# Kernel tuning notes

Measured on AMD Instinct MI355X. Metric: run time of the kernel, lower is better.

Reference implementation:

```python
import jax, jax.numpy as jnp
import numpy as np

N_NODES = 10000
N_EDGES = 640000
MODEL_DIM = 128
HIDDEN = [128, 128]


def setup_inputs() -> dict:
    key = jax.random.key(0)
    ks = jax.random.split(key, 10)
    node_feature = jax.random.normal(ks[0], (N_NODES, MODEL_DIM), dtype=jnp.float32)
    src = jax.random.randint(ks[1], (N_EDGES,), 0, N_NODES, dtype=jnp.int32)
    dst = jax.random.randint(ks[2], (N_EDGES,), 0, N_NODES, dtype=jnp.int32)
    in_dim = 2 * MODEL_DIM  # concat(aggregated_message, node_feature)
    # MLP: in_dim -> 128 -> 128 -> MODEL_DIM, ReLU between hidden layers
    W1 = jax.random.normal(ks[3], (in_dim, HIDDEN[0]), dtype=jnp.float32) / np.sqrt(in_dim)
    b1 = jnp.zeros((HIDDEN[0],), dtype=jnp.float32)
    W2 = jax.random.normal(ks[4], (HIDDEN[0], HIDDEN[1]), dtype=jnp.float32) / np.sqrt(HIDDEN[0])
    b2 = jnp.zeros((HIDDEN[1],), dtype=jnp.float32)
    W3 = jax.random.normal(ks[5], (HIDDEN[1], MODEL_DIM), dtype=jnp.float32) / np.sqrt(HIDDEN[1])
    b3 = jnp.zeros((MODEL_DIM,), dtype=jnp.float32)
    return {"node_feature": node_feature, "src": src, "dst": dst,
            "W1": W1, "b1": b1, "W2": W2, "b2": b2, "W3": W3, "b3": b3}


def reference(node_feature, src, dst, W1, b1, W2, b2, W3, b3):
    # message: gather src node features along edges  [E, D]
    # reduce: sum messages into dst nodes            [N, D]
    agg = jax.ops.segment_sum(node_feature[src], dst, num_segments=N_NODES)
    # apply_node_function_yes_neighbor: concat(aggregated_message, node_feature) -> MLP
    x = jnp.concatenate([agg, node_feature], axis=-1)  # [N, 2D]
    h = jax.nn.relu(x @ W1 + b1)
    h = jax.nn.relu(h @ W2 + b2)
    out = h @ W3 + b3  # [N, D]
    return out
```

## Files before the change

kernel.cpp:

```cpp
#include <hip/hip_runtime.h>
#include <hip/hip_bf16.h>

#define MODEL_D 128
#define CHUNK_SHIFT 13
#define CHUNK_SZ (1 << CHUNK_SHIFT)
#define CAPN 160
#define LDS_HIST 10240

typedef unsigned short ushort_t;
typedef unsigned int uint_t;
typedef __attribute__((ext_vector_type(8))) short short8v;
typedef __attribute__((ext_vector_type(4))) float f32x4;

static __device__ __forceinline__ ushort_t f2b(float v) {
    __hip_bfloat16 h = __float2bfloat16(v);
    return *reinterpret_cast<ushort_t*>(&h);
}

static __device__ __forceinline__ void acc8(float* acc, uint4 wv) {
    union { uint_t u32; float f; } lo, hi;
    lo.u32 = wv.x << 16;          acc[0] += lo.f;
    hi.u32 = wv.x & 0xffff0000u;  acc[1] += hi.f;
    lo.u32 = wv.y << 16;          acc[2] += lo.f;
    hi.u32 = wv.y & 0xffff0000u;  acc[3] += hi.f;
    lo.u32 = wv.z << 16;          acc[4] += lo.f;
    hi.u32 = wv.z & 0xffff0000u;  acc[5] += hi.f;
    lo.u32 = wv.w << 16;          acc[6] += lo.f;
    hi.u32 = wv.w & 0xffff0000u;  acc[7] += hi.f;
}

__global__ __launch_bounds__(1024) void histrank_convert_kernel(
    const int* __restrict__ dst, int* __restrict__ rank,
    int* __restrict__ hist2,
    const float* __restrict__ feat,
    const float* __restrict__ W1, const float* __restrict__ W2,
    const float* __restrict__ W3,
    ushort_t* __restrict__ featB, ushort_t* __restrict__ W1t,
    ushort_t* __restrict__ W2t, ushort_t* __restrict__ W3t,
    int E, int N, int nFeat, int C)
{
    __shared__ int h[LDS_HIST];
    const int t = threadIdx.x;
    const int c = blockIdx.x;

    if (c < C) {
        for (int i = t; i < N; i += 1024) h[i] = 0;
        __syncthreads();
        int e0 = c << CHUNK_SHIFT;
        int e1 = min(e0 + CHUNK_SZ, E);
        for (int e = e0 + t; e < e1; e += 1024)
            rank[e] = atomicAdd(&h[dst[e]], 1);
        __syncthreads();
        for (int i = t; i < N; i += 1024) hist2[(size_t)c * N + i] = h[i];
    }

    int gid = blockIdx.x * 1024 + t;
    int stride = gridDim.x * 1024;
    const int n1 = 256 * 128, n2 = 128 * 128, n3 = 128 * 128;
    int total = nFeat + n1 + n2 + n3;
    for (int i = gid; i < total; i += stride) {
        if (i < nFeat) {
            featB[i] = f2b(feat[i]);
        } else if (i < nFeat + n1) {
            int idx = i - nFeat; int j = idx >> 8, k = idx & 255;
            W1t[idx] = f2b(W1[k * 128 + j]);
        } else if (i < nFeat + n1 + n2) {
            int idx = i - nFeat - n1; int j = idx >> 7, k = idx & 127;
            W2t[idx] = f2b(W2[k * 128 + j]);
        } else {
            int idx = i - nFeat - n1 - n2; int j = idx >> 7, k = idx & 127;
            W3t[idx] = f2b(W3[k * 128 + j]);
        }
    }
}

__global__ __launch_bounds__(1024) void chunkscan_kernel(
    const int* __restrict__ hist2, int* __restrict__ chunkOff,
    int* __restrict__ deg, int N, int C)
{
    int node = blockIdx.x * 1024 + threadIdx.x;
    if (node >= N) return;
    int acc = 0;
    #pragma unroll 4
    for (int c = 0; c < C; ++c) {
        int v = hist2[(size_t)c * N + node];
        chunkOff[(size_t)c * N + node] = acc;
        acc += v;
    }
    deg[node] = acc;
}

__global__ __launch_bounds__(1024) void fill_kernel(
    const int* __restrict__ src, const int* __restrict__ dst,
    const int* __restrict__ rank, const int* __restrict__ chunkOff,
    int* __restrict__ srcSorted, int E, int N)
{
    int gid = blockIdx.x * 1024 + threadIdx.x;
    int stride = gridDim.x * 1024;
    for (int e = gid; e < E; e += stride) {
        int d = dst[e];
        int c = e >> CHUNK_SHIFT;
        int off = chunkOff[(size_t)c * N + d] + rank[e];
        if (off < CAPN) srcSorted[d * CAPN + off] = src[e];
    }
}

__global__ __launch_bounds__(256) void agg_kernel(
    const ushort_t* __restrict__ featB,
    const int* __restrict__ deg, const int* __restrict__ srcSorted,
    ushort_t* __restrict__ aggB, int N)
{
    int gid = blockIdx.x * 256 + threadIdx.x;
    int node = gid >> 6;
    if (node >= N) return;
    int lane = gid & 63;
    const int g4 = lane >> 4;
    const int c16 = lane & 15;
    const size_t cOff = c16 * 8;

    float acc[8];
    #pragma unroll
    for (int j = 0; j < 8; ++j) acc[j] = 0.f;

    int degN = deg[node];
    degN = (degN < CAPN) ? degN : CAPN;
    const int sbase = node * CAPN;

    for (int chunk = 0; chunk < degN; chunk += 64) {
        int e = chunk + lane;
        int myidx = (e < degN) ? srcSorted[sbase + e] : 0;
        int nact = degN - chunk;
        nact = (nact < 64) ? nact : 64;
        int nfull = nact >> 2;

        int u = 0;
        for (; u + 4 <= nfull; u += 4) {
            int s0 = __shfl(myidx, (u + 0) * 4 + g4);
            int s1 = __shfl(myidx, (u + 1) * 4 + g4);
            int s2 = __shfl(myidx, (u + 2) * 4 + g4);
            int s3 = __shfl(myidx, (u + 3) * 4 + g4);
            uint4 wv0 = *(const uint4*)(featB + (size_t)s0 * MODEL_D + cOff);
            uint4 wv1 = *(const uint4*)(featB + (size_t)s1 * MODEL_D + cOff);
            uint4 wv2 = *(const uint4*)(featB + (size_t)s2 * MODEL_D + cOff);
            uint4 wv3 = *(const uint4*)(featB + (size_t)s3 * MODEL_D + cOff);
            acc8(acc, wv0);
            acc8(acc, wv1);
            acc8(acc, wv2);
            acc8(acc, wv3);
        }
        for (; u < nfull; ++u) {
            int s = __shfl(myidx, u * 4 + g4);
            uint4 wv = *(const uint4*)(featB + (size_t)s * MODEL_D + cOff);
            acc8(acc, wv);
        }
        int rem = nact & 3;
        if (rem) {
            bool valid = g4 < rem;
            int sel = valid ? (nfull * 4 + g4) : 0;
            int s = __shfl(myidx, sel);
            uint4 wv = *(const uint4*)(featB + (size_t)s * MODEL_D + cOff);
            if (valid) acc8(acc, wv);
        }
    }

    #pragma unroll
    for (int j = 0; j < 8; ++j) {
        acc[j] += __shfl_xor(acc[j], 16);
        acc[j] += __shfl_xor(acc[j], 32);
    }

    if (lane < 16) {
        uint4 o;
        o.x = (uint_t)f2b(acc[0]) | ((uint_t)f2b(acc[1]) << 16);
        o.y = (uint_t)f2b(acc[2]) | ((uint_t)f2b(acc[3]) << 16);
        o.z = (uint_t)f2b(acc[4]) | ((uint_t)f2b(acc[5]) << 16);
        o.w = (uint_t)f2b(acc[6]) | ((uint_t)f2b(acc[7]) << 16);
        *(uint4*)(aggB + (size_t)node * MODEL_D + c16 * 8) = o;
    }
}

__global__ __launch_bounds__(256) void mlp_kernel(
    const ushort_t* __restrict__ aggB, const ushort_t* __restrict__ featB,
    const ushort_t* __restrict__ W1t, const ushort_t* __restrict__ W2t,
    const ushort_t* __restrict__ W3t,
    const float* __restrict__ b1, const float* __restrict__ b2,
    const float* __restrict__ b3,
    float* __restrict__ out, int N)
{
    __shared__ ushort_t h1[64][136];
    __shared__ ushort_t h2[64][136];

    const int t = threadIdx.x;
    const int lane = t & 63;
    const int w = t >> 6;
    const int r16 = lane & 15;
    const int g = lane >> 4;
    const int nb0 = blockIdx.x * 64;

    {
        short8v B1[2][8];
        float bias1[2];
        #pragma unroll
        for (int cc = 0; cc < 2; ++cc) {
            const int ct = w * 2 + cc;
            #pragma unroll
            for (int ks = 0; ks < 8; ++ks)
                B1[cc][ks] = *(const short8v*)(W1t + (ct * 16 + r16) * 256 + ks * 32 + g * 8);
            bias1[cc] = b1[ct * 16 + r16];
        }
        #pragma unroll
        for (int b = 0; b < 4; ++b) {
            int nodeA = nb0 + b * 16 + r16;
            int nodeAc = (nodeA < N) ? nodeA : (N - 1);
            short8v a1f[8];
            #pragma unroll
            for (int ks = 0; ks < 4; ++ks)
                a1f[ks] = *(const short8v*)(aggB + (size_t)nodeAc * MODEL_D + ks * 32 + g * 8);
            #pragma unroll
            for (int ks = 0; ks < 4; ++ks)
                a1f[4 + ks] = *(const short8v*)(featB + (size_t)nodeAc * MODEL_D + ks * 32 + g * 8);
            #pragma unroll
            for (int cc = 0; cc < 2; ++cc) {
                const int ct = w * 2 + cc;
                f32x4 c = {0.f, 0.f, 0.f, 0.f};
                #pragma unroll
                for (int ks = 0; ks < 8; ++ks)
                    c = __builtin_amdgcn_mfma_f32_16x16x32_bf16(a1f[ks], B1[cc][ks], c, 0, 0, 0);
                #pragma unroll
                for (int i = 0; i < 4; ++i) {
                    float v = fmaxf(c[i] + bias1[cc], 0.f);
                    h1[b * 16 + g * 4 + i][ct * 16 + r16] = f2b(v);
                }
            }
        }
    }
    __syncthreads();

    {
        short8v B2[2][4];
        float bias2[2];
        #pragma unroll
        for (int cc = 0; cc < 2; ++cc) {
            const int ct = w * 2 + cc;
            #pragma unroll
            for (int ks = 0; ks < 4; ++ks)
                B2[cc][ks] = *(const short8v*)(W2t + (ct * 16 + r16) * 128 + ks * 32 + g * 8);
            bias2[cc] = b2[ct * 16 + r16];
        }
        #pragma unroll
        for (int b = 0; b < 4; ++b) {
            short8v a2f[4];
            #pragma unroll
            for (int ks = 0; ks < 4; ++ks)
                a2f[ks] = *(const short8v*)&h1[b * 16 + r16][ks * 32 + g * 8];
            #pragma unroll
            for (int cc = 0; cc < 2; ++cc) {
                const int ct = w * 2 + cc;
                f32x4 c = {0.f, 0.f, 0.f, 0.f};
                #pragma unroll
                for (int ks = 0; ks < 4; ++ks)
                    c = __builtin_amdgcn_mfma_f32_16x16x32_bf16(a2f[ks], B2[cc][ks], c, 0, 0, 0);
                #pragma unroll
                for (int i = 0; i < 4; ++i) {
                    float v = fmaxf(c[i] + bias2[cc], 0.f);
                    h2[b * 16 + g * 4 + i][ct * 16 + r16] = f2b(v);
                }
            }
        }
    }
    __syncthreads();

    {
        short8v B3[2][4];
        float bias3[2];
        #pragma unroll
        for (int cc = 0; cc < 2; ++cc) {
            const int ct = w * 2 + cc;
            #pragma unroll
            for (int ks = 0; ks < 4; ++ks)
                B3[cc][ks] = *(const short8v*)(W3t + (ct * 16 + r16) * 128 + ks * 32 + g * 8);
            bias3[cc] = b3[ct * 16 + r16];
        }
        #pragma unroll
        for (int b = 0; b < 4; ++b) {
            short8v a3f[4];
            #pragma unroll
            for (int ks = 0; ks < 4; ++ks)
                a3f[ks] = *(const short8v*)&h2[b * 16 + r16][ks * 32 + g * 8];
            #pragma unroll
            for (int cc = 0; cc < 2; ++cc) {
                const int ct = w * 2 + cc;
                f32x4 c = {0.f, 0.f, 0.f, 0.f};
                #pragma unroll
                for (int ks = 0; ks < 4; ++ks)
                    c = __builtin_amdgcn_mfma_f32_16x16x32_bf16(a3f[ks], B3[cc][ks], c, 0, 0, 0);
                #pragma unroll
                for (int i = 0; i < 4; ++i) {
                    int node = nb0 + b * 16 + g * 4 + i;
                    if (node < N)
                        out[(size_t)node * MODEL_D + ct * 16 + r16] = c[i] + bias3[cc];
                }
            }
        }
    }
}

extern "C" void kernel_launch(void* const* d_in, const int* in_sizes, int n_in,
                              void* d_out, int out_size, void* d_ws, size_t ws_size,
                              hipStream_t stream) {
    const float* feat = (const float*)d_in[0];
    const int*   src  = (const int*)d_in[1];
    const int*   dst  = (const int*)d_in[2];
    const float* W1   = (const float*)d_in[3];
    const float* b1   = (const float*)d_in[4];
    const float* W2   = (const float*)d_in[5];
    const float* b2   = (const float*)d_in[6];
    const float* W3   = (const float*)d_in[7];
    const float* b3   = (const float*)d_in[8];
    float* out = (float*)d_out;

    const int N = in_sizes[0] / MODEL_D;
    const int E = in_sizes[1];
    const int NFEAT = N * MODEL_D;
    const int C = (E + CHUNK_SZ - 1) >> CHUNK_SHIFT;

    ushort_t* featB = (ushort_t*)d_ws;
    ushort_t* aggB  = featB + NFEAT;
    ushort_t* W1t   = aggB + NFEAT;
    ushort_t* W2t   = W1t + 256 * 128;
    ushort_t* W3t   = W2t + 128 * 128;
    int* rank       = (int*)(W3t + 128 * 128);
    int* hist2      = rank + E;
    int* chunkOff   = hist2 + (size_t)C * N;
    int* deg        = chunkOff + (size_t)C * N;
    int* srcSorted  = deg + N;

    histrank_convert_kernel<<<625, 1024, 0, stream>>>(
        dst, rank, hist2, feat, W1, W2, W3,
        featB, W1t, W2t, W3t, E, N, NFEAT, C);

    chunkscan_kernel<<<(N + 1023) / 1024, 1024, 0, stream>>>(
        hist2, chunkOff, deg, N, C);

    fill_kernel<<<625, 1024, 0, stream>>>(
        src, dst, rank, chunkOff, srcSorted, E, N);

    agg_kernel<<<(N * 64 + 255) / 256, 256, 0, stream>>>(
        featB, deg, srcSorted, aggB, N);

    mlp_kernel<<<(N + 63) / 64, 256, 0, stream>>>(
        aggB, featB, W1t, W2t, W3t, b1, b2, b3, out, N);
}
```

Baseline: 59.94 us.

## Fuse all stages into one cooperative kernel with grid-wide syncs

Merges the five launches (histogram/convert, chunk scan, fill, aggregation, MLP) into a single cooperative kernel of 256 blocks × 1024 threads. Stages are separated by grid.sync() instead of kernel boundaries. The MLP phase is remapped so 16 waves each own one column tile and two row blocks, and the histogram LDS buffer is reused for the MLP intermediates. This aims to remove per-launch overhead and inter-kernel gaps, but adds grid-sync costs, caps occupancy at one large block per CU for the gather phase, and runs every stage under the register limits of a 1024-thread launch.

```diff
diff --git a/kernel.cpp b/kernel.cpp
--- a/kernel.cpp
+++ b/kernel.cpp
@@ -1,11 +1,16 @@
 #include <hip/hip_runtime.h>
 #include <hip/hip_bf16.h>
+#include <hip/hip_cooperative_groups.h>
+
+namespace cg = cooperative_groups;
 
 #define MODEL_D 128
 #define CHUNK_SHIFT 13
 #define CHUNK_SZ (1 << CHUNK_SHIFT)
 #define CAPN 160
 #define LDS_HIST 10240
+#define NBLK 256
+#define NTHR 1024
 
 typedef unsigned short ushort_t;
 typedef unsigned int uint_t;
@@ -29,276 +34,249 @@
     hi.u32 = wv.w & 0xffff0000u;  acc[7] += hi.f;
 }
 
-__global__ __launch_bounds__(1024) void histrank_convert_kernel(
-    const int* __restrict__ dst, int* __restrict__ rank,
-    int* __restrict__ hist2,
+__global__ void __launch_bounds__(NTHR) fused_all(
     const float* __restrict__ feat,
-    const float* __restrict__ W1, const float* __restrict__ W2,
-    const float* __restrict__ W3,
+    const int* __restrict__ src, const int* __restrict__ dst,
+    const float* __restrict__ W1, const float* __restrict__ b1,
+    const float* __restrict__ W2, const float* __restrict__ b2,
+    const float* __restrict__ W3, const float* __restrict__ b3,
     ushort_t* __restrict__ featB, ushort_t* __restrict__ W1t,
     ushort_t* __restrict__ W2t, ushort_t* __restrict__ W3t,
+    int* __restrict__ rank, int* __restrict__ hist2,
+    int* __restrict__ chunkOff, int* __restrict__ deg,
+    int* __restrict__ srcSorted, ushort_t* __restrict__ aggB,
+    float* __restrict__ out,
     int E, int N, int nFeat, int C)
 {
-    __shared__ int h[LDS_HIST];
+    cg::grid_group grid = cg::this_grid();
+    __shared__ int smem[LDS_HIST];
+
     const int t = threadIdx.x;
-    const int c = blockIdx.x;
-
-    if (c < C) {
-        for (int i = t; i < N; i += 1024) h[i] = 0;
+    const int blk = blockIdx.x;
+
+    if (blk < C) {
+        for (int i = t; i < N; i += NTHR) smem[i] = 0;
         __syncthreads();
-        int e0 = c << CHUNK_SHIFT;
+        int e0 = blk << CHUNK_SHIFT;
         int e1 = min(e0 + CHUNK_SZ, E);
-        for (int e = e0 + t; e < e1; e += 1024)
-            rank[e] = atomicAdd(&h[dst[e]], 1);
+        for (int e = e0 + t; e < e1; e += NTHR)
+            rank[e] = atomicAdd(&smem[dst[e]], 1);
         __syncthreads();
-        for (int i = t; i < N; i += 1024) hist2[(size_t)c * N + i] = h[i];
-    }
-
-    int gid = blockIdx.x * 1024 + t;
-    int stride = gridDim.x * 1024;
-    const int n1 = 256 * 128, n2 = 128 * 128, n3 = 128 * 128;
-    int total = nFeat + n1 + n2 + n3;
-    for (int i = gid; i < total; i += stride) {
-        if (i < nFeat) {
-            featB[i] = f2b(feat[i]);
-        } else if (i < nFeat + n1) {
-            int idx = i - nFeat; int j = idx >> 8, k = idx & 255;
-            W1t[idx] = f2b(W1[k * 128 + j]);
-        } else if (i < nFeat + n1 + n2) {
-            int idx = i - nFeat - n1; int j = idx >> 7, k = idx & 127;
-            W2t[idx] = f2b(W2[k * 128 + j]);
-        } else {
-            int idx = i - nFeat - n1 - n2; int j = idx >> 7, k = idx & 127;
-            W3t[idx] = f2b(W3[k * 128 + j]);
-        }
-    }
-}
-
-__global__ __launch_bounds__(1024) void chunkscan_kernel(
-    const int* __restrict__ hist2, int* __restrict__ chunkOff,
-    int* __restrict__ deg, int N, int C)
-{
-    int node = blockIdx.x * 1024 + threadIdx.x;
-    if (node >= N) return;
-    int acc = 0;
-    #pragma unroll 4
-    for (int c = 0; c < C; ++c) {
-        int v = hist2[(size_t)c * N + node];
-        chunkOff[(size_t)c * N + node] = acc;
-        acc += v;
-    }
-    deg[node] = acc;
-}
-
-__global__ __launch_bounds__(1024) void fill_kernel(
-    const int* __restrict__ src, const int* __restrict__ dst,
-    const int* __restrict__ rank, const int* __restrict__ chunkOff,
-    int* __restrict__ srcSorted, int E, int N)
-{
-    int gid = blockIdx.x * 1024 + threadIdx.x;
-    int stride = gridDim.x * 1024;
-    for (int e = gid; e < E; e += stride) {
-        int d = dst[e];
-        int c = e >> CHUNK_SHIFT;
-        int off = chunkOff[(size_t)c * N + d] + rank[e];
-        if (off < CAPN) srcSorted[d * CAPN + off] = src[e];
-    }
-}
-
-__global__ __launch_bounds__(256) void agg_kernel(
-    const ushort_t* __restrict__ featB,
-    const int* __restrict__ deg, const int* __restrict__ srcSorted,
-    ushort_t* __restrict__ aggB, int N)
-{
-    int gid = blockIdx.x * 256 + threadIdx.x;
-    int node = gid >> 6;
-    if (node >= N) return;
-    int lane = gid & 63;
-    const int g4 = lane >> 4;
-    const int c16 = lane & 15;
-    const size_t cOff = c16 * 8;
-
-    float acc[8];
-    #pragma unroll
-    for (int j = 0; j < 8; ++j) acc[j] = 0.f;
-
-    int degN = deg[node];
-    degN = (degN < CAPN) ? degN : CAPN;
-    const int sbase = node * CAPN;
-
-    for (int chunk = 0; chunk < degN; chunk += 64) {
-        int e = chunk + lane;
-        int myidx = (e < degN) ? srcSorted[sbase + e] : 0;
-        int nact = degN - chunk;
-        nact = (nact < 64) ? nact : 64;
-        int nfull = nact >> 2;
-
-        int u = 0;
-        for (; u + 4 <= nfull; u += 4) {
-            int s0 = __shfl(myidx, (u + 0) * 4 + g4);
-            int s1 = __shfl(myidx, (u + 1) * 4 + g4);
-            int s2 = __shfl(myidx, (u + 2) * 4 + g4);
-            int s3 = __shfl(myidx, (u + 3) * 4 + g4);
-            uint4 wv0 = *(const uint4*)(featB + (size_t)s0 * MODEL_D + cOff);
-            uint4 wv1 = *(const uint4*)(featB + (size_t)s1 * MODEL_D + cOff);
-            uint4 wv2 = *(const uint4*)(featB + (size_t)s2 * MODEL_D + cOff);
-            uint4 wv3 = *(const uint4*)(featB + (size_t)s3 * MODEL_D + cOff);
-            acc8(acc, wv0);
-            acc8(acc, wv1);
-            acc8(acc, wv2);
-            acc8(acc, wv3);
-        }
-        for (; u < nfull; ++u) {
-            int s = __shfl(myidx, u * 4 + g4);
-            uint4 wv = *(const uint4*)(featB + (size_t)s * MODEL_D + cOff);
-            acc8(acc, wv);
-        }
-        int rem = nact & 3;
-        if (rem) {
-            bool valid = g4 < rem;
-            int sel = valid ? (nfull * 4 + g4) : 0;
-            int s = __shfl(myidx, sel);
-            uint4 wv = *(const uint4*)(featB + (size_t)s * MODEL_D + cOff);
-            if (valid) acc8(acc, wv);
-        }
-    }
-
-    #pragma unroll
-    for (int j = 0; j < 8; ++j) {
-        acc[j] += __shfl_xor(acc[j], 16);
-        acc[j] += __shfl_xor(acc[j], 32);
-    }
-
-    if (lane < 16) {
-        uint4 o;
-        o.x = (uint_t)f2b(acc[0]) | ((uint_t)f2b(acc[1]) << 16);
-        o.y = (uint_t)f2b(acc[2]) | ((uint_t)f2b(acc[3]) << 16);
-        o.z = (uint_t)f2b(acc[4]) | ((uint_t)f2b(acc[5]) << 16);
-        o.w = (uint_t)f2b(acc[6]) | ((uint_t)f2b(acc[7]) << 16);
-        *(uint4*)(aggB + (size_t)node * MODEL_D + c16 * 8) = o;
-    }
-}
-
-__global__ __launch_bounds__(256) void mlp_kernel(
-    const ushort_t* __restrict__ aggB, const ushort_t* __restrict__ featB,
-    const ushort_t* __restrict__ W1t, const ushort_t* __restrict__ W2t,
-    const ushort_t* __restrict__ W3t,
-    const float* __restrict__ b1, const float* __restrict__ b2,
-    const float* __restrict__ b3,
-    float* __restrict__ out, int N)
-{
-    __shared__ ushort_t h1[64][136];
-    __shared__ ushort_t h2[64][136];
-
-    const int t = threadIdx.x;
-    const int lane = t & 63;
-    const int w = t >> 6;
-    const int r16 = lane & 15;
-    const int g = lane >> 4;
-    const int nb0 = blockIdx.x * 64;
-
-    {
-        short8v B1[2][8];
-        float bias1[2];
-        #pragma unroll
-        for (int cc = 0; cc < 2; ++cc) {
-            const int ct = w * 2 + cc;
+        for (int i = t; i < N; i += NTHR) hist2[(size_t)blk * N + i] = smem[i];
+    }
+    {
+        int gid = blk * NTHR + t;
+        int stride = NBLK * NTHR;
+        const int n1 = 256 * 128, n2 = 128 * 128, n3 = 128 * 128;
+        int total = nFeat + n1 + n2 + n3;
+        for (int i = gid; i < total; i += stride) {
+            if (i < nFeat) {
+                featB[i] = f2b(feat[i]);
+            } else if (i < nFeat + n1) {
+                int idx = i - nFeat; int j = idx >> 8, k = idx & 255;
+                W1t[idx] = f2b(W1[k * 128 + j]);
+            } else if (i < nFeat + n1 + n2) {
+                int idx = i - nFeat - n1; int j = idx >> 7, k = idx & 127;
+                W2t[idx] = f2b(W2[k * 128 + j]);
+            } else {
+                int idx = i - nFeat - n1 - n2; int j = idx >> 7, k = idx & 127;
+                W3t[idx] = f2b(W3[k * 128 + j]);
+            }
+        }
+    }
+    grid.sync();
+
+    {
+        int node = blk * NTHR + t;
+        if (node < N) {
+            int acc = 0;
+            #pragma unroll 4
+            for (int c = 0; c < C; ++c) {
+                int v = hist2[(size_t)c * N + node];
+                chunkOff[(size_t)c * N + node] = acc;
+                acc += v;
+            }
+            deg[node] = acc;
+        }
+    }
+    grid.sync();
+
+    {
+        int gid = blk * NTHR + t;
+        int stride = NBLK * NTHR;
+        for (int e = gid; e < E; e += stride) {
+            int d = dst[e];
+            int c = e >> CHUNK_SHIFT;
+            int off = chunkOff[(size_t)c * N + d] + rank[e];
+            if (off < CAPN) srcSorted[d * CAPN + off] = src[e];
+        }
+    }
+    grid.sync();
+
+    {
+        const int lane = t & 63;
+        const int g4 = lane >> 4;
+        const int c16 = lane & 15;
+        const size_t cOff = c16 * 8;
+        int gw = blk * (NTHR / 64) + (t >> 6);
+        for (int node = gw; node < N; node += NBLK * (NTHR / 64)) {
+            float acc[8];
             #pragma unroll
-            for (int ks = 0; ks < 8; ++ks)
-                B1[cc][ks] = *(const short8v*)(W1t + (ct * 16 + r16) * 256 + ks * 32 + g * 8);
-            bias1[cc] = b1[ct * 16 + r16];
-        }
-        #pragma unroll
-        for (int b = 0; b < 4; ++b) {
-            int nodeA = nb0 + b * 16 + r16;
-            int nodeAc = (nodeA < N) ? nodeA : (N - 1);
-            short8v a1f[8];
+            for (int j = 0; j < 8; ++j) acc[j] = 0.f;
+
+            int degN = deg[node];
+            degN = (degN < CAPN) ? degN : CAPN;
+            const int sbase = node * CAPN;
+
+            for (int chunk = 0; chunk < degN; chunk += 64) {
+                int e = chunk + lane;
+                int myidx = (e < degN) ? srcSorted[sbase + e] : 0;
+                int nact = degN - chunk;
+                nact = (nact < 64) ? nact : 64;
+                int nfull = nact >> 2;
+
+                int u = 0;
+                for (; u + 4 <= nfull; u += 4) {
+                    int s0 = __shfl(myidx, (u + 0) * 4 + g4);
+                    int s1 = __shfl(myidx, (u + 1) * 4 + g4);
+                    int s2 = __shfl(myidx, (u + 2) * 4 + g4);
+                    int s3 = __shfl(myidx, (u + 3) * 4 + g4);
+                    uint4 wv0 = *(const uint4*)(featB + (size_t)s0 * MODEL_D + cOff);
+                    uint4 wv1 = *(const uint4*)(featB + (size_t)s1 * MODEL_D + cOff);
+                    uint4 wv2 = *(const uint4*)(featB + (size_t)s2 * MODEL_D + cOff);
+                    uint4 wv3 = *(const uint4*)(featB + (size_t)s3 * MODEL_D + cOff);
+                    acc8(acc, wv0);
+                    acc8(acc, wv1);
+                    acc8(acc, wv2);
+                    acc8(acc, wv3);
+                }
+                for (; u < nfull; ++u) {
+                    int s = __shfl(myidx, u * 4 + g4);
+                    uint4 wv = *(const uint4*)(featB + (size_t)s * MODEL_D + cOff);
+                    acc8(acc, wv);
+                }
+                int rem = nact & 3;
+                if (rem) {
+                    bool valid = g4 < rem;
+                    int sel = valid ? (nfull * 4 + g4) : 0;
+                    int s = __shfl(myidx, sel);
+                    uint4 wv = *(const uint4*)(featB + (size_t)s * MODEL_D + cOff);
+                    if (valid) acc8(acc, wv);
+                }
+            }
+
             #pragma unroll
-            for (int ks = 0; ks < 4; ++ks)
-                a1f[ks] = *(const short8v*)(aggB + (size_t)nodeAc * MODEL_D + ks * 32 + g * 8);
-            #pragma unroll
-            for (int ks = 0; ks < 4; ++ks)
-                a1f[4 + ks] = *(const short8v*)(featB + (size_t)nodeAc * MODEL_D + ks * 32 + g * 8);
-            #pragma unroll
-            for (int cc = 0; cc < 2; ++cc) {
-                const int ct = w * 2 + cc;
-                f32x4 c = {0.f, 0.f, 0.f, 0.f};
+            for (int j = 0; j < 8; ++j) {
+                acc[j] += __shfl_xor(acc[j], 16);
+                acc[j] += __shfl_xor(acc[j], 32);
+            }
+
+            if (lane < 16) {
+                uint4 o;
+                o.x = (uint_t)f2b(acc[0]) | ((uint_t)f2b(acc[1]) << 16);
+                o.y = (uint_t)f2b(acc[2]) | ((uint_t)f2b(acc[3]) << 16);
+                o.z = (uint_t)f2b(acc[4]) | ((uint_t)f2b(acc[5]) << 16);
+                o.w = (uint_t)f2b(acc[6]) | ((uint_t)f2b(acc[7]) << 16);
+                *(uint4*)(aggB + (size_t)node * MODEL_D + c16 * 8) = o;
+            }
+        }
+    }
+    grid.sync();
+
+    {
+        const int ntiles = (N + 63) / 64;
+        if (blk < ntiles) {
+            ushort_t (*h1)[136] = reinterpret_cast<ushort_t(*)[136]>(smem);
+            ushort_t (*h2)[136] = h1 + 64;
+
+            const int lane = t & 63;
+            const int w = t >> 6;
+            const int r16 = lane & 15;
+            const int g = lane >> 4;
+            const int nb0 = blk * 64;
+            const int ct = w >> 1;
+            const int bh = w & 1;
+
+            {
+                short8v B1[8];
                 #pragma unroll
                 for (int ks = 0; ks < 8; ++ks)
-                    c = __builtin_amdgcn_mfma_f32_16x16x32_bf16(a1f[ks], B1[cc][ks], c, 0, 0, 0);
-                #pragma unroll
-                for (int i = 0; i < 4; ++i) {
-                    float v = fmaxf(c[i] + bias1[cc], 0.f);
-                    h1[b * 16 + g * 4 + i][ct * 16 + r16] = f2b(v);
-                }
-            }
-        }
-    }
-    __syncthreads();
-
-    {
-        short8v B2[2][4];
-        float bias2[2];
-        #pragma unroll
-        for (int cc = 0; cc < 2; ++cc) {
-            const int ct = w * 2 + cc;
-            #pragma unroll
-            for (int ks = 0; ks < 4; ++ks)
-                B2[cc][ks] = *(const short8v*)(W2t + (ct * 16 + r16) * 128 + ks * 32 + g * 8);
-            bias2[cc] = b2[ct * 16 + r16];
-        }
-        #pragma unroll
-        for (int b = 0; b < 4; ++b) {
-            short8v a2f[4];
-            #pragma unroll
-            for (int ks = 0; ks < 4; ++ks)
-                a2f[ks] = *(const short8v*)&h1[b * 16 + r16][ks * 32 + g * 8];
-            #pragma unroll
-            for (int cc = 0; cc < 2; ++cc) {
-                const int ct = w * 2 + cc;
-                f32x4 c = {0.f, 0.f, 0.f, 0.f};
+                    B1[ks] = *(const short8v*)(W1t + (ct * 16 + r16) * 256 + ks * 32 + g * 8);
+                float bias1 = b1[ct * 16 + r16];
+                #pragma unroll
+                for (int bi = 0; bi < 2; ++bi) {
+                    int b = bh * 2 + bi;
+                    int nodeA = nb0 + b * 16 + r16;
+                    int nodeAc = (nodeA < N) ? nodeA : (N - 1);
+                    short8v a1f[8];
+                    #pragma unroll
+                    for (int ks = 0; ks < 4; ++ks)
+                        a1f[ks] = *(const short8v*)(aggB + (size_t)nodeAc * MODEL_D + ks * 32 + g * 8);
+                    #pragma unroll
+                    for (int ks = 0; ks < 4; ++ks)
+                        a1f[4 + ks] = *(const short8v*)(featB + (size_t)nodeAc * MODEL_D + ks * 32 + g * 8);
+                    f32x4 c = {0.f, 0.f, 0.f, 0.f};
+                    #pragma unroll
+                    for (int ks = 0; ks < 8; ++ks)
+                        c = __builtin_amdgcn_mfma_f32_16x16x32_bf16(a1f[ks], B1[ks], c, 0, 0, 0);
+                    #pragma unroll
+                    for (int i = 0; i < 4; ++i) {
+                        float v = fmaxf(c[i] + bias1, 0.f);
+                        h1[b * 16 + g * 4 + i][ct * 16 + r16] = f2b(v);
+                    }
+                }
+            }
+            __syncthreads();
+
+            {
+                short8v B2[4];
                 #pragma unroll
                 for (int ks = 0; ks < 4; ++ks)
-                    c = __builtin_amdgcn_mfma_f32_16x16x32_bf16(a2f[ks], B2[cc][ks], c, 0, 0, 0);
-                #pragma unroll
-                for (int i = 0; i < 4; ++i) {
-                    float v = fmaxf(c[i] + bias2[cc], 0.f);
-                    h2[b * 16 + g * 4 + i][ct * 16 + r16] = f2b(v);
-                }
-            }
-        }
-    }
-    __syncthreads();
-
-    {
-        short8v B3[2][4];
-        float bias3[2];
-        #pragma unroll
-        for (int cc = 0; cc < 2; ++cc) {
-            const int ct = w * 2 + cc;
-            #pragma unroll
-            for (int ks = 0; ks < 4; ++ks)
-                B3[cc][ks] = *(const short8v*)(W3t + (ct * 16 + r16) * 128 + ks * 32 + g * 8);
-            bias3[cc] = b3[ct * 16 + r16];
-        }
-        #pragma unroll
-        for (int b = 0; b < 4; ++b) {
-            short8v a3f[4];
-            #pragma unroll
-            for (int ks = 0; ks < 4; ++ks)
-                a3f[ks] = *(const short8v*)&h2[b * 16 + r16][ks * 32 + g * 8];
-            #pragma unroll
-            for (int cc = 0; cc < 2; ++cc) {
-                const int ct = w * 2 + cc;
-                f32x4 c = {0.f, 0.f, 0.f, 0.f};
+                    B2[ks] = *(const short8v*)(W2t + (ct * 16 + r16) * 128 + ks * 32 + g * 8);
+                float bias2 = b2[ct * 16 + r16];
+                #pragma unroll
+                for (int bi = 0; bi < 2; ++bi) {
+                    int b = bh * 2 + bi;
+                    short8v a2f[4];
+                    #pragma unroll
+                    for (int ks = 0; ks < 4; ++ks)
+                        a2f[ks] = *(const short8v*)&h1[b * 16 + r16][ks * 32 + g * 8];
+                    f32x4 c = {0.f, 0.f, 0.f, 0.f};
+                    #pragma unroll
+                    for (int ks = 0; ks < 4; ++ks)
+                        c = __builtin_amdgcn_mfma_f32_16x16x32_bf16(a2f[ks], B2[ks], c, 0, 0, 0);
+                    #pragma unroll
+                    for (int i = 0; i < 4; ++i) {
+                        float v = fmaxf(c[i] + bias2, 0.f);
+                        h2[b * 16 + g * 4 + i][ct * 16 + r16] = f2b(v);
+                    }
+                }
+            }
+            __syncthreads();
+
+            {
+                short8v B3[4];
                 #pragma unroll
                 for (int ks = 0; ks < 4; ++ks)
-                    c = __builtin_amdgcn_mfma_f32_16x16x32_bf16(a3f[ks], B3[cc][ks], c, 0, 0, 0);
-                #pragma unroll
-                for (int i = 0; i < 4; ++i) {
-                    int node = nb0 + b * 16 + g * 4 + i;
-                    if (node < N)
-                        out[(size_t)node * MODEL_D + ct * 16 + r16] = c[i] + bias3[cc];
+                    B3[ks] = *(const short8v*)(W3t + (ct * 16 + r16) * 128 + ks * 32 + g * 8);
+                float bias3 = b3[ct * 16 + r16];
+                #pragma unroll
+                for (int bi = 0; bi < 2; ++bi) {
+                    int b = bh * 2 + bi;
+                    short8v a3f[4];
+                    #pragma unroll
+                    for (int ks = 0; ks < 4; ++ks)
+                        a3f[ks] = *(const short8v*)&h2[b * 16 + r16][ks * 32 + g * 8];
+                    f32x4 c = {0.f, 0.f, 0.f, 0.f};
+                    #pragma unroll
+                    for (int ks = 0; ks < 4; ++ks)
+                        c = __builtin_amdgcn_mfma_f32_16x16x32_bf16(a3f[ks], B3[ks], c, 0, 0, 0);
+                    #pragma unroll
+                    for (int i = 0; i < 4; ++i) {
+                        int node = nb0 + b * 16 + g * 4 + i;
+                        if (node < N)
+                            out[(size_t)node * MODEL_D + ct * 16 + r16] = c[i] + bias3;
+                    }
                 }
             }
         }
@@ -319,10 +297,10 @@
     const float* b3   = (const float*)d_in[8];
     float* out = (float*)d_out;
 
-    const int N = in_sizes[0] / MODEL_D;
-    const int E = in_sizes[1];
-    const int NFEAT = N * MODEL_D;
-    const int C = (E + CHUNK_SZ - 1) >> CHUNK_SHIFT;
+    int N = in_sizes[0] / MODEL_D;
+    int E = in_sizes[1];
+    int NFEAT = N * MODEL_D;
+    int C = (E + CHUNK_SZ - 1) >> CHUNK_SHIFT;
 
     ushort_t* featB = (ushort_t*)d_ws;
     ushort_t* aggB  = featB + NFEAT;
@@ -335,19 +313,14 @@
     int* deg        = chunkOff + (size_t)C * N;
     int* srcSorted  = deg + N;
 
-    histrank_convert_kernel<<<625, 1024, 0, stream>>>(
-        dst, rank, hist2, feat, W1, W2, W3,
-        featB, W1t, W2t, W3t, E, N, NFEAT, C);
-
-    chunkscan_kernel<<<(N + 1023) / 1024, 1024, 0, stream>>>(
-        hist2, chunkOff, deg, N, C);
-
-    fill_kernel<<<625, 1024, 0, stream>>>(
-        src, dst, rank, chunkOff, srcSorted, E, N);
-
-    agg_kernel<<<(N * 64 + 255) / 256, 256, 0, stream>>>(
-        featB, deg, srcSorted, aggB, N);
-
-    mlp_kernel<<<(N + 63) / 64, 256, 0, stream>>>(
-        aggB, featB, W1t, W2t, W3t, b1, b2, b3, out, N);
+    void* args[] = {
+        (void*)&feat, (void*)&src, (void*)&dst,
+        (void*)&W1, (void*)&b1, (void*)&W2, (void*)&b2, (void*)&W3, (void*)&b3,
+        (void*)&featB, (void*)&W1t, (void*)&W2t, (void*)&W3t,
+        (void*)&rank, (void*)&hist2, (void*)&chunkOff, (void*)&deg,
+        (void*)&srcSorted, (void*)&aggB, (void*)&out,
+        (void*)&E, (void*)&N, (void*)&NFEAT, (void*)&C
+    };
+    hipLaunchCooperativeKernel((void*)fused_all, dim3(NBLK), dim3(NTHR),
+                               args, 0, stream);
 }
```

New measurement: 203.8 us. +240.0%, slower.
